# Optimization experiments

Hardware: AMD Instinct MI355X
Metric: run time of the kernel (lower is better)

Reference implementation:

```python
import jax, jax.numpy as jnp
import numpy as np

B, CIN, K, H, W = 8, 256, 128, 112, 112


def setup_inputs() -> dict:
    key = jax.random.key(0)
    k1, k2, k3, k4 = jax.random.split(key, 4)
    return {
        "x": jax.random.normal(k1, (B, CIN, H, W), jnp.float32),
        "linComb": jax.random.uniform(k2, (K, CIN), dtype=jnp.float32),
        "geoParams": jax.random.uniform(k3, (K, 2, 3), dtype=jnp.float32),
        "boxParams": jax.random.uniform(k4, (K, 2, 3), dtype=jnp.float32),
    }


def _affine_sample(img, theta):
    """F.affine_grid + F.grid_sample (bilinear, zeros padding, align_corners=False).
    img: [B, K, H, W] (one feature channel per geometric channel k)
    theta: [K, 2, 3] affine params, shared across batch.
    """
    Bn, Kn, Hn, Wn = img.shape
    # normalized output coords (align_corners=False pixel centers)
    xs = (2.0 * jnp.arange(Wn, dtype=img.dtype) + 1.0) / Wn - 1.0
    ys = (2.0 * jnp.arange(Hn, dtype=img.dtype) + 1.0) / Hn - 1.0
    gxv, gyv = jnp.meshgrid(xs, ys)  # [H, W]
    coords = jnp.stack([gxv, gyv, jnp.ones_like(gxv)], axis=-1)  # [H, W, 3]
    grid = jnp.einsum('kij,hwj->khwi', theta, coords)  # [K, H, W, 2] (x, y)
    # unnormalize to input pixel space
    ix = ((grid[..., 0] + 1.0) * Wn - 1.0) * 0.5
    iy = ((grid[..., 1] + 1.0) * Hn - 1.0) * 0.5
    x0 = jnp.floor(ix)
    y0 = jnp.floor(iy)
    wx1 = ix - x0
    wx0 = 1.0 - wx1
    wy1 = iy - y0
    wy0 = 1.0 - wy1
    imgf = img.reshape(Bn, Kn, Hn * Wn)

    def gather(xc, yc, w):
        valid = (xc >= 0) & (xc <= Wn - 1) & (yc >= 0) & (yc <= Hn - 1)
        xi = jnp.clip(xc, 0, Wn - 1).astype(jnp.int32)
        yi = jnp.clip(yc, 0, Hn - 1).astype(jnp.int32)
        idx = (yi * Wn + xi).reshape(Kn, Hn * Wn)
        vals = jnp.take_along_axis(
            imgf, jnp.broadcast_to(idx[None], (Bn, Kn, Hn * Wn)), axis=2
        ).reshape(Bn, Kn, Hn, Wn)
        return vals * (w * valid.astype(img.dtype))[None]

    out = (gather(x0, y0, wx0 * wy0)
           + gather(x0 + 1.0, y0, wx1 * wy0)
           + gather(x0, y0 + 1.0, wx0 * wy1)
           + gather(x0 + 1.0, y0 + 1.0, wx1 * wy1))
    return out


def reference(x, linComb, geoParams, boxParams):
    # channel-weighted sum: (x.unsqueeze(1) * linComb).sum(dim=2) == 1x1-conv GEMM
    comb = jnp.einsum('bchw,kc->bkhw', x, linComb)  # [B, K, H, W]
    box = _affine_sample(jnp.ones_like(comb), boxParams)
    warped = _affine_sample(comb, geoParams)
    finalPred = warped * box
    return (finalPred, warped, box)
```

## Files before the change

### kernel.cpp

```cpp
#include <hip/hip_runtime.h>

namespace {
constexpr int Bn = 8, Cn = 256, Kn = 128, Hn = 112, Wn = 112;
constexpr int Pn = Hn * Wn;
constexpr long long NOUT = (long long)Bn * Kn * Pn;
}

__global__ __launch_bounds__(256) void transpose_lc(const float* __restrict__ lc,
                                                    float* __restrict__ lcT) {
  int i = blockIdx.x * 256 + threadIdx.x;
  int c = i >> 7, k = i & 127;
  lcT[i] = lc[k * Cn + c];
}

__global__ __launch_bounds__(256) void gemm_comb(const float* __restrict__ x,
                                                 const float* __restrict__ lcT,
                                                 float* __restrict__ comb) {
  __shared__ __align__(16) float xs[8][128];
  __shared__ __align__(16) float ls[8][128];
  const int tid = threadIdx.x;
  const int b = blockIdx.x / 98;
  const int pbase = (blockIdx.x % 98) * 128;
  const int kbase = (tid >> 5) * 16;
  const int ploc = (tid & 31) * 4;

  const int s_cc = tid >> 5;
  const int s_e4 = (tid & 31) * 4;

  float acc[16][4];
#pragma unroll
  for (int i = 0; i < 16; ++i)
#pragma unroll
    for (int j = 0; j < 4; ++j) acc[i][j] = 0.f;

  const float* xb = x + (size_t)b * Cn * Pn + pbase;

  for (int cb = 0; cb < Cn; cb += 8) {
    float4 xv4 = *reinterpret_cast<const float4*>(&xb[(size_t)(cb + s_cc) * Pn + s_e4]);
    float4 lv4 = *reinterpret_cast<const float4*>(&lcT[(cb + s_cc) * Kn + s_e4]);
    *reinterpret_cast<float4*>(&xs[s_cc][s_e4]) = xv4;
    *reinterpret_cast<float4*>(&ls[s_cc][s_e4]) = lv4;
    __syncthreads();
#pragma unroll
    for (int cc = 0; cc < 8; ++cc) {
      float4 xv = *reinterpret_cast<const float4*>(&xs[cc][ploc]);
      float xa[4] = {xv.x, xv.y, xv.z, xv.w};
#pragma unroll
      for (int i4 = 0; i4 < 4; ++i4) {
        float4 lv = *reinterpret_cast<const float4*>(&ls[cc][kbase + i4 * 4]);
        float la[4] = {lv.x, lv.y, lv.z, lv.w};
#pragma unroll
        for (int ii = 0; ii < 4; ++ii) {
          const int i = i4 * 4 + ii;
#pragma unroll
          for (int j = 0; j < 4; ++j) acc[i][j] += la[ii] * xa[j];
        }
      }
    }
    __syncthreads();
  }

  float* co = comb + (size_t)b * Kn * Pn + pbase + ploc;
#pragma unroll
  for (int i = 0; i < 16; ++i) {
    float4 v = make_float4(acc[i][0], acc[i][1], acc[i][2], acc[i][3]);
    *reinterpret_cast<float4*>(&co[(size_t)(kbase + i) * Pn]) = v;
  }
}

template <int FUSE>
__global__ __launch_bounds__(256) void sample_all(const float* __restrict__ comb,
                                                  const float* __restrict__ geo,
                                                  const float* __restrict__ boxp,
                                                  float* __restrict__ outF,
                                                  float* __restrict__ outW,
                                                  float* __restrict__ outB) {
  const int k = blockIdx.y;
  const int p = blockIdx.x * 256 + threadIdx.x;
  const int h = p / Wn;
  const int w = p - h * Wn;
  const float xn = (2.f * w + 1.f) / (float)Wn - 1.f;
  const float yn = (2.f * h + 1.f) / (float)Hn - 1.f;

  const float* g = geo + k * 6;
  const float* t = boxp + k * 6;

  float ix = ((g[0] * xn + g[1] * yn + g[2] + 1.f) * Wn - 1.f) * 0.5f;
  float iy = ((g[3] * xn + g[4] * yn + g[5] + 1.f) * Hn - 1.f) * 0.5f;
  float x0f = floorf(ix), y0f = floorf(iy);
  float wx1 = ix - x0f, wx0 = 1.f - wx1;
  float wy1 = iy - y0f, wy0 = 1.f - wy1;
  float vx0 = (x0f >= 0.f && x0f <= (float)(Wn - 1)) ? 1.f : 0.f;
  float vx1 = (x0f + 1.f >= 0.f && x0f + 1.f <= (float)(Wn - 1)) ? 1.f : 0.f;
  float vy0 = (y0f >= 0.f && y0f <= (float)(Hn - 1)) ? 1.f : 0.f;
  float vy1 = (y0f + 1.f >= 0.f && y0f + 1.f <= (float)(Hn - 1)) ? 1.f : 0.f;
  int x0i = (int)fminf(fmaxf(x0f, 0.f), (float)(Wn - 1));
  int x1i = (int)fminf(fmaxf(x0f + 1.f, 0.f), (float)(Wn - 1));
  int y0i = (int)fminf(fmaxf(y0f, 0.f), (float)(Hn - 1));
  int y1i = (int)fminf(fmaxf(y0f + 1.f, 0.f), (float)(Hn - 1));
  float w00 = wx0 * wy0 * vx0 * vy0;
  float w01 = wx1 * wy0 * vx1 * vy0;
  float w10 = wx0 * wy1 * vx0 * vy1;
  float w11 = wx1 * wy1 * vx1 * vy1;
  int i00 = y0i * Wn + x0i, i01 = y0i * Wn + x1i;
  int i10 = y1i * Wn + x0i, i11 = y1i * Wn + x1i;

  float bix = ((t[0] * xn + t[1] * yn + t[2] + 1.f) * Wn - 1.f) * 0.5f;
  float biy = ((t[3] * xn + t[4] * yn + t[5] + 1.f) * Hn - 1.f) * 0.5f;
  float bx0 = floorf(bix), by0 = floorf(biy);
  float bwx1 = bix - bx0, bwx0 = 1.f - bwx1;
  float bwy1 = biy - by0, bwy0 = 1.f - bwy1;
  float bvx0 = (bx0 >= 0.f && bx0 <= (float)(Wn - 1)) ? 1.f : 0.f;
  float bvx1 = (bx0 + 1.f >= 0.f && bx0 + 1.f <= (float)(Wn - 1)) ? 1.f : 0.f;
  float bvy0 = (by0 >= 0.f && by0 <= (float)(Hn - 1)) ? 1.f : 0.f;
  float bvy1 = (by0 + 1.f >= 0.f && by0 + 1.f <= (float)(Hn - 1)) ? 1.f : 0.f;
  float bv = bwx0 * bwy0 * bvx0 * bvy0 + bwx1 * bwy0 * bvx1 * bvy0 +
             bwx0 * bwy1 * bvx0 * bvy1 + bwx1 * bwy1 * bvx1 * bvy1;

#pragma unroll
  for (int b = 0; b < Bn; ++b) {
    const float* cp = comb + ((size_t)b * Kn + k) * Pn;
    float v = w00 * cp[i00] + w01 * cp[i01] + w10 * cp[i10] + w11 * cp[i11];
    size_t o = ((size_t)b * Kn + k) * Pn + p;
    outW[o] = v;
    outB[o] = bv;
    if (FUSE) outF[o] = v * bv;
  }
}

__global__ __launch_bounds__(256) void mul_fw(const float* __restrict__ w,
                                              const float* __restrict__ bx,
                                              float* __restrict__ f) {
  const long long n4 = NOUT / 4;
  for (long long i = blockIdx.x * 256LL + threadIdx.x; i < n4;
       i += (long long)gridDim.x * 256LL) {
    float4 a = reinterpret_cast<const float4*>(w)[i];
    float4 b = reinterpret_cast<const float4*>(bx)[i];
    reinterpret_cast<float4*>(f)[i] = make_float4(a.x * b.x, a.y * b.y, a.z * b.z, a.w * b.w);
  }
}

extern "C" void kernel_launch(void* const* d_in, const int* in_sizes, int n_in,
                              void* d_out, int out_size, void* d_ws, size_t ws_size,
                              hipStream_t stream) {
  (void)in_sizes; (void)n_in; (void)out_size;
  const float* x = (const float*)d_in[0];
  const float* lc = (const float*)d_in[1];
  const float* geo = (const float*)d_in[2];
  const float* boxp = (const float*)d_in[3];
  float* outF = (float*)d_out;
  float* outW = outF + NOUT;
  float* outB = outW + NOUT;

  const size_t comb_bytes = (size_t)NOUT * sizeof(float);
  const bool use_ws = ws_size >= comb_bytes;
  float* comb = use_ws ? (float*)d_ws : outF;
  float* lcT = outB;

  transpose_lc<<<(Kn * Cn) / 256, 256, 0, stream>>>(lc, lcT);
  gemm_comb<<<Bn * (Pn / 128), 256, 0, stream>>>(x, lcT, comb);
  if (use_ws) {
    sample_all<1><<<dim3(Pn / 256, Kn), 256, 0, stream>>>(comb, geo, boxp, outF, outW, outB);
  } else {
    sample_all<0><<<dim3(Pn / 256, Kn), 256, 0, stream>>>(comb, geo, boxp, outF, outW, outB);
    mul_fw<<<2048, 256, 0, stream>>>(outW, outB, outF);
  }
}
```

Baseline: 334.2 us.

## Use bf16 MFMA for channel GEMM and store intermediate comb in bf16

Replaces the FP32 shared-memory FMA GEMM with a matrix-core kernel that converts x and linComb to bf16 in registers and calls mfma_f32_16x16x32_bf16, loading operands straight from global memory with no LDS staging. The linComb prep now packs pairs of bf16 values in a single-block kernel. The intermediate comb tensor is stored as bf16, which halves its write and gather traffic in the sampling kernel. This cuts compute and memory cost but lowers precision to bf16 for a K=256 reduction, which risks exceeding tolerance, and the uncoalesced strided x loads may limit bandwidth.

Measured after the change: 308.4 us. 7.7% less time.

```diff
diff --git a/kernel.cpp b/kernel.cpp
--- a/kernel.cpp
+++ b/kernel.cpp
@@ -1,75 +1,99 @@
 #include <hip/hip_runtime.h>
+#include <hip/hip_bf16.h>
 
 namespace {
 constexpr int Bn = 8, Cn = 256, Kn = 128, Hn = 112, Wn = 112;
 constexpr int Pn = Hn * Wn;
 constexpr long long NOUT = (long long)Bn * Kn * Pn;
+
+typedef __attribute__((ext_vector_type(8))) short bf16x8;
+typedef __attribute__((ext_vector_type(4))) float f32x4;
+
+__device__ inline unsigned short f2bf(float f) {
+  __hip_bfloat16 h = __float2bfloat16(f);
+  return __builtin_bit_cast(unsigned short, h);
+}
+__device__ inline unsigned int pack2bf(float a, float b) {
+  return (unsigned int)f2bf(a) | ((unsigned int)f2bf(b) << 16);
+}
+__device__ inline float bf2f(unsigned short u) {
+  return __bfloat162float(__builtin_bit_cast(__hip_bfloat16, u));
+}
 }
 
-__global__ __launch_bounds__(256) void transpose_lc(const float* __restrict__ lc,
-                                                    float* __restrict__ lcT) {
-  int i = blockIdx.x * 256 + threadIdx.x;
-  int c = i >> 7, k = i & 127;
-  lcT[i] = lc[k * Cn + c];
+__global__ __launch_bounds__(256) void prep_lcP(const float* __restrict__ lc,
+                                                unsigned int* __restrict__ lcP) {
+  for (int i = 0; i < 64; ++i) {
+    int idx = threadIdx.x + 256 * (blockIdx.x * 64 + i);
+    if (idx < 128 * 128) {
+      int c2 = idx >> 7, k = idx & 127;
+      lcP[idx] = pack2bf(lc[k * Cn + 2 * c2], lc[k * Cn + 2 * c2 + 1]);
+    }
+  }
 }
 
-__global__ __launch_bounds__(256) void gemm_comb(const float* __restrict__ x,
-                                                 const float* __restrict__ lcT,
-                                                 float* __restrict__ comb) {
-  __shared__ __align__(16) float xs[8][128];
-  __shared__ __align__(16) float ls[8][128];
+__global__ __launch_bounds__(256) void gemm_mfma(const float* __restrict__ x,
+                                                 const unsigned int* __restrict__ lcP,
+                                                 unsigned short* __restrict__ combh) {
   const int tid = threadIdx.x;
+  const int wid = tid >> 6;
+  const int lane = tid & 63;
+  const int l15 = lane & 15, l4 = lane >> 4;
   const int b = blockIdx.x / 98;
-  const int pbase = (blockIdx.x % 98) * 128;
-  const int kbase = (tid >> 5) * 16;
-  const int ploc = (tid & 31) * 4;
+  const int p0 = (blockIdx.x % 98) * 128 + wid * 32;
+  const float* xb = x + (size_t)b * Cn * Pn;
 
-  const int s_cc = tid >> 5;
-  const int s_e4 = (tid & 31) * 4;
+  f32x4 acc[8][2];
+#pragma unroll
+  for (int ks = 0; ks < 8; ++ks)
+#pragma unroll
+    for (int ps = 0; ps < 2; ++ps) acc[ks][ps] = (f32x4)(0.f);
 
-  float acc[16][4];
+#pragma unroll 2
+  for (int s = 0; s < 8; ++s) {
+    unsigned int a[2][4];
 #pragma unroll
-  for (int i = 0; i < 16; ++i)
+    for (int ps = 0; ps < 2; ++ps) {
+      const float* src = xb + (size_t)(32 * s + l4 * 8) * Pn + (p0 + ps * 16 + l15);
+      float v[8];
 #pragma unroll
-    for (int j = 0; j < 4; ++j) acc[i][j] = 0.f;
-
-  const float* xb = x + (size_t)b * Cn * Pn + pbase;
-
-  for (int cb = 0; cb < Cn; cb += 8) {
-    float4 xv4 = *reinterpret_cast<const float4*>(&xb[(size_t)(cb + s_cc) * Pn + s_e4]);
-    float4 lv4 = *reinterpret_cast<const float4*>(&lcT[(cb + s_cc) * Kn + s_e4]);
-    *reinterpret_cast<float4*>(&xs[s_cc][s_e4]) = xv4;
-    *reinterpret_cast<float4*>(&ls[s_cc][s_e4]) = lv4;
-    __syncthreads();
+      for (int j = 0; j < 8; ++j) v[j] = src[(size_t)j * Pn];
 #pragma unroll
-    for (int cc = 0; cc < 8; ++cc) {
-      float4 xv = *reinterpret_cast<const float4*>(&xs[cc][ploc]);
-      float xa[4] = {xv.x, xv.y, xv.z, xv.w};
+      for (int r = 0; r < 4; ++r) a[ps][r] = pack2bf(v[2 * r], v[2 * r + 1]);
+    }
 #pragma unroll
-      for (int i4 = 0; i4 < 4; ++i4) {
-        float4 lv = *reinterpret_cast<const float4*>(&ls[cc][kbase + i4 * 4]);
-        float la[4] = {lv.x, lv.y, lv.z, lv.w};
+    for (int ks = 0; ks < 8; ++ks) {
+      unsigned int bf[4];
+      const unsigned int* bp = lcP + (16 * s + l4 * 4) * 128 + ks * 16 + l15;
 #pragma unroll
-        for (int ii = 0; ii < 4; ++ii) {
-          const int i = i4 * 4 + ii;
+      for (int r = 0; r < 4; ++r) bf[r] = bp[r * 128];
+      union { unsigned int u[4]; bf16x8 v; } bu;
+      bu.u[0] = bf[0]; bu.u[1] = bf[1]; bu.u[2] = bf[2]; bu.u[3] = bf[3];
 #pragma unroll
-          for (int j = 0; j < 4; ++j) acc[i][j] += la[ii] * xa[j];
-        }
+      for (int ps = 0; ps < 2; ++ps) {
+        union { unsigned int u[4]; bf16x8 v; } au;
+        au.u[0] = a[ps][0]; au.u[1] = a[ps][1]; au.u[2] = a[ps][2]; au.u[3] = a[ps][3];
+        acc[ks][ps] = __builtin_amdgcn_mfma_f32_16x16x32_bf16(au.v, bu.v, acc[ks][ps], 0, 0, 0);
       }
     }
-    __syncthreads();
   }
 
-  float* co = comb + (size_t)b * Kn * Pn + pbase + ploc;
 #pragma unroll
-  for (int i = 0; i < 16; ++i) {
-    float4 v = make_float4(acc[i][0], acc[i][1], acc[i][2], acc[i][3]);
-    *reinterpret_cast<float4*>(&co[(size_t)(kbase + i) * Pn]) = v;
+  for (int ks = 0; ks < 8; ++ks) {
+    const size_t krow = ((size_t)b * Kn + ks * 16 + l15) * Pn;
+#pragma unroll
+    for (int ps = 0; ps < 2; ++ps) {
+      const int p = p0 + ps * 16 + l4 * 4;
+      uint2 st;
+      st.x = pack2bf(acc[ks][ps][0], acc[ks][ps][1]);
+      st.y = pack2bf(acc[ks][ps][2], acc[ks][ps][3]);
+      *reinterpret_cast<uint2*>(combh + krow + p) = st;
+    }
   }
 }
 
 template <int FUSE>
-__global__ __launch_bounds__(256) void sample_all(const float* __restrict__ comb,
+__global__ __launch_bounds__(256) void sample_all(const unsigned short* __restrict__ comb,
                                                   const float* __restrict__ geo,
                                                   const float* __restrict__ boxp,
                                                   float* __restrict__ outF,
@@ -119,8 +143,9 @@
 
 #pragma unroll
   for (int b = 0; b < Bn; ++b) {
-    const float* cp = comb + ((size_t)b * Kn + k) * Pn;
-    float v = w00 * cp[i00] + w01 * cp[i01] + w10 * cp[i10] + w11 * cp[i11];
+    const unsigned short* cp = comb + ((size_t)b * Kn + k) * Pn;
+    float v = w00 * bf2f(cp[i00]) + w01 * bf2f(cp[i01]) +
+              w10 * bf2f(cp[i10]) + w11 * bf2f(cp[i11]);
     size_t o = ((size_t)b * Kn + k) * Pn + p;
     outW[o] = v;
     outB[o] = bv;
@@ -152,17 +177,18 @@
   float* outW = outF + NOUT;
   float* outB = outW + NOUT;
 
-  const size_t comb_bytes = (size_t)NOUT * sizeof(float);
+  unsigned int* lcP = (unsigned int*)outB;
+
+  const size_t comb_bytes = (size_t)NOUT * sizeof(unsigned short);
   const bool use_ws = ws_size >= comb_bytes;
-  float* comb = use_ws ? (float*)d_ws : outF;
-  float* lcT = outB;
+  unsigned short* combh = use_ws ? (unsigned short*)d_ws : (unsigned short*)outF;
 
-  transpose_lc<<<(Kn * Cn) / 256, 256, 0, stream>>>(lc, lcT);
-  gemm_comb<<<Bn * (Pn / 128), 256, 0, stream>>>(x, lcT, comb);
+  prep_lcP<<<1, 256, 0, stream>>>(lc, lcP);
+  gemm_mfma<<<Bn * (Pn / 128), 256, 0, stream>>>(x, lcP, combh);
   if (use_ws) {
-    sample_all<1><<<dim3(Pn / 256, Kn), 256, 0, stream>>>(comb, geo, boxp, outF, outW, outB);
+    sample_all<1><<<dim3(Pn / 256, Kn), 256, 0, stream>>>(combh, geo, boxp, outF, outW, outB);
   } else {
-    sample_all<0><<<dim3(Pn / 256, Kn), 256, 0, stream>>>(comb, geo, boxp, outF, outW, outB);
+    sample_all<0><<<dim3(Pn / 256, Kn), 256, 0, stream>>>(combh, geo, boxp, outF, outW, outB);
     mul_fw<<<2048, 256, 0, stream>>>(outW, outB, outF);
   }
 }
```
